# Kernel tuning notes

Measured on AMD Instinct MI355X. Metric: run time of the kernel, lower is better.

## Reference

```python
import jax, jax.numpy as jnp
from jax import lax
import numpy as np

N_POINTS = 1_000_000
K_STEPS = 32
N_FUNCS = 8
H = W = 1024
FID = 1000


def setup_inputs() -> dict:
    key = jax.random.key(0)
    ks = jax.random.split(key, 8)
    # palette: monotone 4-channel colormap-like table in [0,1]
    palette = jax.random.uniform(ks[0], (FID, 4), dtype=jnp.float32)
    # contractive-ish affine IFS so points stay mostly in frame
    A = 0.6 * jax.random.normal(ks[1], (N_FUNCS, 2, 2), dtype=jnp.float32)
    b = 0.8 * jax.random.normal(ks[2], (N_FUNCS, 2), dtype=jnp.float32)
    fcolor = jax.random.uniform(ks[3], (N_FUNCS,), dtype=jnp.float32)
    xy0 = jax.random.normal(ks[4], (N_POINTS, 2), dtype=jnp.float32)  # Normal(0, initial_sigma=1)
    c0 = jax.random.uniform(ks[5], (N_POINTS, 1), dtype=jnp.float32)
    fn_idx = jax.random.randint(ks[6], (K_STEPS, N_POINTS), 0, N_FUNCS, dtype=jnp.int32)
    # frame: x_left=-2, x_right=2, y_top=-2, y_bottom=2
    min_vec = jnp.array([[-2.0, -2.0]], dtype=jnp.float32)
    range_vec = jnp.array([[W / 4.0, H / 4.0]], dtype=jnp.float32)
    raw_image = jnp.zeros((4, H, W), dtype=jnp.float32)
    return {"raw_image": raw_image, "palette": palette, "A": A, "b": b,
            "fcolor": fcolor, "xy0": xy0, "c0": c0, "min_vec": min_vec,
            "range_vec": range_vec, "fn_idx": fn_idx, "skip_first_k": 4}


def reference(raw_image, palette, A, b, fcolor, xy0, c0, min_vec, range_vec, fn_idx, skip_first_k):
    height, width = raw_image.shape[1], raw_image.shape[2]
    fid = palette.shape[0]
    k_steps = fn_idx.shape[0]

    def step(carry, scanned):
        xy, c, img = carry
        idx, k = scanned
        # FunctionSet: per-point affine map + color blend
        xy = jnp.einsum('nij,nj->ni', A[idx], xy) + b[idx]          # [N,2]
        c = (c + fcolor[idx][:, None]) * 0.5                        # [N,1]
        colors = c[:, 0]
        pal_idx = (colors * (fid - 1) + 0.5 / fid).astype(jnp.int32)
        color_vectors = palette[jnp.clip(pal_idx, 0, fid - 1)]      # [N,4]
        bins = ((xy - min_vec) * range_vec).astype(jnp.int32)       # trunc toward 0, like .long()
        x_bins, y_bins = bins[:, 0], bins[:, 1]
        in_bounds = ((x_bins >= 0) & (x_bins < width) &
                     (y_bins >= 0) & (y_bins < height) & (k >= skip_first_k))
        vals = jnp.where(in_bounds[:, None], color_vectors, 0.0)    # [N,4]
        xb = jnp.clip(x_bins, 0, height - 1)  # source indexes img[c][x_bins, y_bins]
        yb = jnp.clip(y_bins, 0, width - 1)
        img = img.at[:, xb, yb].add(vals.T)
        return (xy, c, img), None

    (_, _, img), _ = lax.scan(step, (xy0, c0, raw_image),
                              (fn_idx, jnp.arange(k_steps)))
    return img
```

## Files before the change

### kernel.cpp

```cpp
#include <hip/hip_runtime.h>

typedef unsigned int u32;
typedef unsigned long long u64;

#define NPTS   1000000
#define KSTEPS 32
#define NF     8
#define IMG_H  1024
#define IMG_W  1024
#define FID    1000
#define HW     (IMG_H * IMG_W)
#define NB     3907
#define NBKT   512
#define BKTPX  2048
#define SEGW   (256 * KSTEPS)
#define K5G    1024
#define PARTCH 1016
#define PARTA_CH 488
#define MSTG   512
#define FPSCALE 4194304.0f
#define FPINV   (1.0f / 4194304.0f)

#define GETIDX(K)                                                              \
    ((int)(((((K) >> 3) == 0 ? p0 : ((K) >> 3) == 1 ? p1                       \
            : ((K) >> 3) == 2 ? p2 : p3) >> (((K) & 7) * 4)) & 7u))

#define FLAME_STEP(IDX, K)                                                     \
  {                                                                            \
    const float a00 = s_tab[(IDX)*8+0], a01 = s_tab[(IDX)*8+1];                \
    const float a10 = s_tab[(IDX)*8+2], a11 = s_tab[(IDX)*8+3];                \
    const float b0  = s_tab[(IDX)*8+4], b1  = s_tab[(IDX)*8+5];                \
    const float fc  = s_tab[(IDX)*8+6];                                        \
    const float nx = __fadd_rn(__fadd_rn(__fmul_rn(a00,x),__fmul_rn(a01,y)),b0);\
    const float ny = __fadd_rn(__fadd_rn(__fmul_rn(a10,x),__fmul_rn(a11,y)),b1);\
    x = nx; y = ny;                                                            \
    c = __fmul_rn(__fadd_rn(c, fc), 0.5f);                                     \
    xb = (int)__fmul_rn(__fsub_rn(x, minx), rx);                               \
    yb = (int)__fmul_rn(__fsub_rn(y, miny), ry);                               \
    inb = (xb >= 0) & (xb < IMG_W) & (yb >= 0) & (yb < IMG_H) & ((K) >= skipk);\
  }

#define LOAD_TABLES()                                                          \
    if (threadIdx.x < NF) {                                                    \
        const int f = threadIdx.x;                                             \
        s_tab[f*8+0] = Amat[f*4+0]; s_tab[f*8+1] = Amat[f*4+1];                \
        s_tab[f*8+2] = Amat[f*4+2]; s_tab[f*8+3] = Amat[f*4+3];                \
        s_tab[f*8+4] = bvec[f*2+0]; s_tab[f*8+5] = bvec[f*2+1];                \
        s_tab[f*8+6] = fcolor[f];   s_tab[f*8+7] = 0.0f;                       \
    }

__device__ __forceinline__ u32* part_ptr(u32* partA, u32* partB, u32 w) {
    return (w < PARTA_CH) ? partA + (size_t)w * (BKTPX * 4)
                          : partB + (size_t)(w - PARTA_CH) * (BKTPX * 4);
}
__device__ __forceinline__ const u32* part_ptr_c(const u32* partA,
                                                 const u32* partB, u32 w) {
    return (w < PARTA_CH) ? partA + (size_t)w * (BKTPX * 4)
                          : partB + (size_t)(w - PARTA_CH) * (BKTPX * 4);
}

__global__ __launch_bounds__(256) void k_flame(
    const float* __restrict__ Amat, const float* __restrict__ bvec,
    const float* __restrict__ fcolor,
    const float* __restrict__ xy0, const float* __restrict__ c0,
    const float* __restrict__ minv, const float* __restrict__ rangev,
    const int* __restrict__ fn_idx, const int* __restrict__ skipk_ptr,
    u32* __restrict__ counts, u32* __restrict__ lpre,
    u32* __restrict__ blockmajor)
{
    __shared__ u32 s_rec[SEGW];
    __shared__ u32 s_cnt[NBKT];
    __shared__ u32 s_scan[256];
    __shared__ float s_tab[NF * 8];
    const int tid = threadIdx.x;

    s_cnt[tid] = 0u; s_cnt[tid + 256] = 0u;
    LOAD_TABLES();
    __syncthreads();

    const int i = blockIdx.x * 256 + tid;
    u32 rec[KSTEPS];

    if (i < NPTS) {
        u32 p0 = 0, p1 = 0, p2 = 0, p3 = 0;
        #pragma unroll
        for (int k = 0; k < 8; ++k)
            p0 |= ((u32)fn_idx[(size_t)k * NPTS + i] & 7u) << (k * 4);
        #pragma unroll
        for (int k = 0; k < 8; ++k)
            p1 |= ((u32)fn_idx[(size_t)(k + 8) * NPTS + i] & 7u) << (k * 4);
        #pragma unroll
        for (int k = 0; k < 8; ++k)
            p2 |= ((u32)fn_idx[(size_t)(k + 16) * NPTS + i] & 7u) << (k * 4);
        #pragma unroll
        for (int k = 0; k < 8; ++k)
            p3 |= ((u32)fn_idx[(size_t)(k + 24) * NPTS + i] & 7u) << (k * 4);

        const int   skipk = skipk_ptr[0];
        const float minx = minv[0], miny = minv[1];
        const float rx = rangev[0], ry = rangev[1];
        const float2 xyv = ((const float2*)xy0)[i];
        float x = xyv.x, y = xyv.y, c = c0[i];
        #pragma unroll
        for (int k = 0; k < KSTEPS; ++k) {
            const int idx = GETIDX(k);
            int xb, yb; bool inb;
            FLAME_STEP(idx, k);
            u32 r = 0xFFFFFFFFu;
            if (inb) {
                int pi = (int)__fadd_rn(__fmul_rn(c, 999.0f), 0.0005f);
                pi = min(max(pi, 0), FID - 1);
                r = (((u32)(xb << 10 | yb)) << 10) | (u32)pi;
                atomicAdd(&s_cnt[r >> 21], 1u);
            }
            rec[k] = r;
        }
    }
    __syncthreads();

    const u32 cA = s_cnt[2 * tid], cB = s_cnt[2 * tid + 1];
    const u32 psum = cA + cB;
    s_scan[tid] = psum; __syncthreads();
    #pragma unroll
    for (int o = 1; o < 256; o <<= 1) {
        u32 t = (tid >= o) ? s_scan[tid - o] : 0u;
        __syncthreads();
        s_scan[tid] += t;
        __syncthreads();
    }
    const u32 excl = s_scan[tid] - psum;

    s_cnt[2 * tid] = excl; s_cnt[2 * tid + 1] = excl + cA;
    const size_t g0 = (size_t)blockIdx.x * NBKT;
    lpre[g0 + 2 * tid] = excl;  lpre[g0 + 2 * tid + 1] = excl + cA;
    counts[g0 + 2 * tid] = cA;  counts[g0 + 2 * tid + 1] = cB;
    __syncthreads();

    if (i < NPTS) {
        #pragma unroll
        for (int k = 0; k < KSTEPS; ++k) {
            const u32 r = rec[k];
            if (r != 0xFFFFFFFFu) {
                const u32 pos = atomicAdd(&s_cnt[r >> 21], 1u);
                s_rec[pos] = r;
            }
        }
    }
    __syncthreads();

    const u32 vt = s_scan[255];
    u32* dst = blockmajor + (size_t)blockIdx.x * SEGW;
    const u32 nv4 = vt >> 2;
    for (u32 q = tid; q < nv4; q += 256)
        ((uint4*)dst)[q] = make_uint4(s_rec[4*q], s_rec[4*q+1],
                                      s_rec[4*q+2], s_rec[4*q+3]);
    for (u32 j = (nv4 << 2) + tid; j < vt; j += 256) dst[j] = s_rec[j];
}

__global__ __launch_bounds__(256) void k_transpose(
    const u32* __restrict__ counts, const u32* __restrict__ lpre,
    u32* __restrict__ counts_t, u32* __restrict__ lpre_t,
    u32* __restrict__ totals)
{
    const int b = blockIdx.x, tid = threadIdx.x;
    u32 s = 0;
    for (int row = tid; row < NB; row += 256) {
        const u32 cv = counts[(size_t)row * NBKT + b];
        const u32 lv = lpre[(size_t)row * NBKT + b];
        counts_t[(size_t)b * NB + row] = cv;
        lpre_t[(size_t)b * NB + row] = lv;
        s += cv;
    }
    __shared__ u32 red[256];
    red[tid] = s; __syncthreads();
    #pragma unroll
    for (int o = 128; o; o >>= 1) {
        if (tid < o) red[tid] += red[tid + o];
        __syncthreads();
    }
    if (tid == 0) totals[b] = red[0];
}

__global__ __launch_bounds__(512) void k_meta(
    const float* __restrict__ palette,
    const u32* __restrict__ totals,
    u32* __restrict__ mm, u32* __restrict__ wstart,
    u32* __restrict__ pal_u32)
{
    __shared__ u32 sc[NBKT];
    const int tid = threadIdx.x;

    for (int t = tid; t < FID * 4; t += 512)
        pal_u32[t] = __float2uint_rn(__fmul_rn(palette[t], FPSCALE));

    const u32 t0 = totals[tid];
    sc[tid] = t0; __syncthreads();
    #pragma unroll
    for (int o = 1; o < NBKT; o <<= 1) {
        u32 v = (tid >= o) ? sc[tid - o] : 0u;
        __syncthreads(); sc[tid] += v; __syncthreads();
    }
    const u32 total = sc[NBKT - 1];

    const u32 m = 1u + (total ? (u32)((504ull * t0) / total) : 0u);
    mm[tid] = m;
    __syncthreads(); sc[tid] = m; __syncthreads();
    #pragma unroll
    for (int o = 1; o < NBKT; o <<= 1) {
        u32 v = (tid >= o) ? sc[tid - o] : 0u;
        __syncthreads(); sc[tid] += v; __syncthreads();
    }
    wstart[tid] = sc[tid] - m;
    if (tid == NBKT - 1) wstart[NBKT] = sc[NBKT - 1];
}

__global__ __launch_bounds__(512) void k_accum(
    const u32* __restrict__ pal_u32,
    const u32* __restrict__ counts_t, const u32* __restrict__ lpre_t,
    const u32* __restrict__ mm, const u32* __restrict__ wstart,
    const u32* __restrict__ blockmajor,
    u32* __restrict__ partA, u32* __restrict__ partB)
{
    __shared__ u64 tileA[BKTPX];
    __shared__ u64 tileB[BKTPX];
    __shared__ u32 s_ml[MSTG];
    __shared__ u32 s_pfx[MSTG + 1];
    __shared__ u32 s_ws[NBKT + 1];
    const int tid = threadIdx.x, w = blockIdx.x;

    if (tid < NBKT) s_ws[tid] = wstart[tid];
    if (tid == 0)   s_ws[NBKT] = wstart[NBKT];
    __syncthreads();
    if ((u32)w >= s_ws[NBKT]) return;

    int b = 0;
    #pragma unroll
    for (int step = 256; step; step >>= 1)
        if (b + step <= NBKT - 1 && s_ws[b + step] <= (u32)w) b += step;

    for (int t = tid; t < BKTPX; t += 512) { tileA[t] = 0ull; tileB[t] = 0ull; }

    const u32 m = mm[b], cch = (u32)w - s_ws[b];
    const u32 gs = (u32)(((u64)NB * cch) / m);
    const u32 ge = (u32)(((u64)NB * (cch + 1)) / m);

    const uint4* pal4 = (const uint4*)pal_u32;
    const u32* ct = counts_t + (size_t)b * NB;
    const u32* lt = lpre_t + (size_t)b * NB;

    for (u32 g0 = gs; g0 < ge; g0 += MSTG) {
        const u32 nm = min((u32)MSTG, ge - g0);
        __syncthreads();
        const u32 myc = (tid < (int)nm) ? ct[g0 + tid] : 0u;
        if (tid < (int)nm) s_ml[tid] = lt[g0 + tid];
        s_pfx[tid + 1] = myc;
        if (tid == 0) s_pfx[0] = 0u;
        __syncthreads();
        #pragma unroll
        for (int o = 1; o < MSTG; o <<= 1) {
            const u32 v = (tid >= o) ? s_pfx[tid - o + 1] : 0u;
            __syncthreads();
            s_pfx[tid + 1] += v;
            __syncthreads();
        }
        const u32 R = s_pfx[MSTG];

        u32 idx = (u32)tid;
        u32 r_c = 0;
        if (idx < R) {
            u32 g = 0;
            #pragma unroll
            for (int step = 256; step; step >>= 1)
                if (s_pfx[g + step] <= idx) g += step;
            r_c = blockmajor[(size_t)(g0 + g) * SEGW + s_ml[g] +
                             (idx - s_pfx[g])];
        }
        while (idx < R) {
            const u32 nidx = idx + 512;
            u32 r_n = 0;
            if (nidx < R) {
                u32 g = 0;
                #pragma unroll
                for (int step = 256; step; step >>= 1)
                    if (s_pfx[g + step] <= nidx) g += step;
                r_n = blockmajor[(size_t)(g0 + g) * SEGW + s_ml[g] +
                                 (nidx - s_pfx[g])];
            }
            const uint4 pc = pal4[r_c & 1023u];
            const u32 local = (r_c >> 10) & (BKTPX - 1);
            atomicAdd(&tileA[local], (u64)pc.x | ((u64)pc.y << 32));
            atomicAdd(&tileB[local], (u64)pc.z | ((u64)pc.w << 32));
            idx = nidx; r_c = r_n;
        }
    }
    __syncthreads();

    uint4* dst = (uint4*)part_ptr(partA, partB, (u32)w);
    for (int t = tid; t < BKTPX; t += 512)
        dst[t] = make_uint4((u32)tileA[t], (u32)(tileA[t] >> 32),
                            (u32)tileB[t], (u32)(tileB[t] >> 32));
}

__global__ __launch_bounds__(256) void k_final(
    const u32* __restrict__ partA, const u32* __restrict__ partB,
    const u32* __restrict__ wstart,
    const float* __restrict__ raw, float* __restrict__ out)
{
    const int p = blockIdx.x * 256 + threadIdx.x;
    const int b = p >> 11, local = p & (BKTPX - 1);
    u32 a0 = 0, a1 = 0, a2 = 0, a3 = 0;
    const u32 w0 = wstart[b], w1 = wstart[b + 1];
    for (u32 w = w0; w < w1; ++w) {
        const uint4 v = ((const uint4*)part_ptr_c(partA, partB, w))[local];
        a0 += v.x; a1 += v.y; a2 += v.z; a3 += v.w;
    }
    out[0*(size_t)HW + p] = __fadd_rn(raw[0*(size_t)HW + p], __fmul_rn((float)a0, FPINV));
    out[1*(size_t)HW + p] = __fadd_rn(raw[1*(size_t)HW + p], __fmul_rn((float)a1, FPINV));
    out[2*(size_t)HW + p] = __fadd_rn(raw[2*(size_t)HW + p], __fmul_rn((float)a2, FPINV));
    out[3*(size_t)HW + p] = __fadd_rn(raw[3*(size_t)HW + p], __fmul_rn((float)a3, FPINV));
}

__global__ __launch_bounds__(256) void flame_accum_packed(
    const float* __restrict__ palette,
    const float* __restrict__ Amat, const float* __restrict__ bvec,
    const float* __restrict__ fcolor,
    const float* __restrict__ xy0, const float* __restrict__ c0,
    const float* __restrict__ minv, const float* __restrict__ rangev,
    const int* __restrict__ fn_idx, const int* __restrict__ skipk_ptr,
    u64* __restrict__ ws)
{
    __shared__ __align__(16) float s_pal[FID * 4];
    __shared__ float s_tab[NF * 8];
    for (int t = threadIdx.x; t < FID; t += 256)
        ((float4*)s_pal)[t] = ((const float4*)palette)[t];
    LOAD_TABLES();
    __syncthreads();

    const int i = blockIdx.x * 256 + threadIdx.x;
    if (i >= NPTS) return;
    const int   skipk = skipk_ptr[0];
    const float minx = minv[0], miny = minv[1];
    const float rx = rangev[0], ry = rangev[1];
    const float2 xyv = ((const float2*)xy0)[i];
    float x = xyv.x, y = xyv.y, c = c0[i];
    for (int k = 0; k < KSTEPS; ++k) {
        const int idx = fn_idx[(size_t)k * NPTS + i];
        int xb, yb; bool inb;
        FLAME_STEP(idx, k);
        if (inb) {
            int pi = (int)__fadd_rn(__fmul_rn(c, 999.0f), 0.0005f);
            pi = min(max(pi, 0), FID - 1);
            const float4 col = *(const float4*)&s_pal[pi * 4];
            const u32 u0 = __float2uint_rn(__fmul_rn(col.x, FPSCALE));
            const u32 u1 = __float2uint_rn(__fmul_rn(col.y, FPSCALE));
            const u32 u2 = __float2uint_rn(__fmul_rn(col.z, FPSCALE));
            const u32 u3 = __float2uint_rn(__fmul_rn(col.w, FPSCALE));
            u64* p = ws + ((size_t)xb * IMG_W + yb) * 2;
            atomicAdd(p + 0, (u64)u0 | ((u64)u1 << 32));
            atomicAdd(p + 1, (u64)u2 | ((u64)u3 << 32));
        }
    }
}

__global__ __launch_bounds__(256) void reduce_packed(
    const u64* __restrict__ ws, const float* __restrict__ raw_image,
    float* __restrict__ out)
{
    const int p = blockIdx.x * 256 + threadIdx.x;
    if (p >= HW) return;
    const u64 w0 = ws[(size_t)p * 2 + 0];
    const u64 w1 = ws[(size_t)p * 2 + 1];
    out[0*(size_t)HW+p] = raw_image[0*(size_t)HW+p] + (float)(u32)(w0 & 0xffffffffull) * FPINV;
    out[1*(size_t)HW+p] = raw_image[1*(size_t)HW+p] + (float)(u32)(w0 >> 32)           * FPINV;
    out[2*(size_t)HW+p] = raw_image[2*(size_t)HW+p] + (float)(u32)(w1 & 0xffffffffull) * FPINV;
    out[3*(size_t)HW+p] = raw_image[3*(size_t)HW+p] + (float)(u32)(w1 >> 32)           * FPINV;
}

extern "C" void kernel_launch(void* const* d_in, const int* in_sizes, int n_in,
                              void* d_out, int out_size, void* d_ws, size_t ws_size,
                              hipStream_t stream) {
    const float* raw_image = (const float*)d_in[0];
    const float* palette   = (const float*)d_in[1];
    const float* A         = (const float*)d_in[2];
    const float* b         = (const float*)d_in[3];
    const float* fcolor    = (const float*)d_in[4];
    const float* xy0       = (const float*)d_in[5];
    const float* c0        = (const float*)d_in[6];
    const float* minv      = (const float*)d_in[7];
    const float* rangev    = (const float*)d_in[8];
    const int*   fn_idx    = (const int*)d_in[9];
    const int*   skipk     = (const int*)d_in[10];
    float* img = (float*)d_out;

    u32* ws = (u32*)d_ws;
    const size_t NBG = (size_t)NB * NBKT;
    u32* counts     = ws;
    u32* lpre       = counts + NBG;
    u32* counts_t   = lpre + NBG;
    u32* lpre_t     = counts_t + NBG;
    u32* totals     = lpre_t + NBG;
    u32* mm         = totals + NBKT;
    u32* wstart     = mm + NBKT;
    u32* pal_u32    = wstart + 1024;
    u32* blockmajor = pal_u32 + 4096;
    u32* partB      = blockmajor + (size_t)NB * SEGW;
    u32* partA      = counts;
    const size_t need_u32 = (size_t)(partB - ws) +
                            (size_t)(PARTCH - PARTA_CH) * (BKTPX * 4);
    const size_t NEED = need_u32 * sizeof(u32);

    if (ws_size >= NEED) {
        k_flame<<<dim3(NB), 256, 0, stream>>>(A, b, fcolor, xy0, c0, minv,
                                              rangev, fn_idx, skipk,
                                              counts, lpre, blockmajor);
        k_transpose<<<dim3(NBKT), 256, 0, stream>>>(counts, lpre,
                                                    counts_t, lpre_t, totals);
        k_meta<<<dim3(1), 512, 0, stream>>>(palette, totals, mm, wstart,
                                            pal_u32);
        k_accum<<<dim3(K5G), 512, 0, stream>>>(pal_u32, counts_t, lpre_t, mm,
                                               wstart, blockmajor,
                                               partA, partB);
        k_final<<<dim3(HW / 256), 256, 0, stream>>>(partA, partB, wstart,
                                                    raw_image, img);
    } else {
        const size_t need2 = (size_t)HW * 2 * sizeof(u64);
        hipMemsetAsync(d_ws, 0, need2, stream);
        flame_accum_packed<<<dim3(NB), 256, 0, stream>>>(
            palette, A, b, fcolor, xy0, c0, minv, rangev, fn_idx, skipk,
            (u64*)d_ws);
        reduce_packed<<<dim3((HW + 255) / 256), 256, 0, stream>>>(
            (const u64*)d_ws, raw_image, img);
    }
}
```

Measured before the change: 182.8 us.

## Split accumulation blocks by channel pair to halve LDS tiles and double grid

Each k_accum chunk now runs as two blocks, each handling two of the four color channels with a single u64 LDS tile instead of two. The grid doubles to 2048 and the partial tiles are stored per half, with k_final reading two uint2 partials per chunk. The aim is to halve LDS use per block for higher occupancy and more parallelism, at the cost of reading and binary-searching the record stream twice.

```diff
diff --git a/kernel.cpp b/kernel.cpp
--- a/kernel.cpp
+++ b/kernel.cpp
@@ -14,9 +14,11 @@
 #define NBKT   512
 #define BKTPX  2048
 #define SEGW   (256 * KSTEPS)
-#define K5G    1024
 #define PARTCH 1016
-#define PARTA_CH 488
+#define HTILES (2 * PARTCH)
+#define HTW    4096
+#define PARTA_T 976
+#define K5G2   2048
 #define MSTG   512
 #define FPSCALE 4194304.0f
 #define FPINV   (1.0f / 4194304.0f)
@@ -49,14 +51,14 @@
         s_tab[f*8+6] = fcolor[f];   s_tab[f*8+7] = 0.0f;                       \
     }
 
-__device__ __forceinline__ u32* part_ptr(u32* partA, u32* partB, u32 w) {
-    return (w < PARTA_CH) ? partA + (size_t)w * (BKTPX * 4)
-                          : partB + (size_t)(w - PARTA_CH) * (BKTPX * 4);
-}
-__device__ __forceinline__ const u32* part_ptr_c(const u32* partA,
-                                                 const u32* partB, u32 w) {
-    return (w < PARTA_CH) ? partA + (size_t)w * (BKTPX * 4)
-                          : partB + (size_t)(w - PARTA_CH) * (BKTPX * 4);
+__device__ __forceinline__ u32* htile_ptr(u32* partA, u32* partB, u32 h) {
+    return (h < PARTA_T) ? partA + (size_t)h * HTW
+                         : partB + (size_t)(h - PARTA_T) * HTW;
+}
+__device__ __forceinline__ const u32* htile_ptr_c(const u32* partA,
+                                                  const u32* partB, u32 h) {
+    return (h < PARTA_T) ? partA + (size_t)h * HTW
+                         : partB + (size_t)(h - PARTA_T) * HTW;
 }
 
 __global__ __launch_bounds__(256) void k_flame(
@@ -221,12 +223,14 @@
     const u32* __restrict__ blockmajor,
     u32* __restrict__ partA, u32* __restrict__ partB)
 {
-    __shared__ u64 tileA[BKTPX];
-    __shared__ u64 tileB[BKTPX];
+    __shared__ u64 tileH[BKTPX];
     __shared__ u32 s_ml[MSTG];
     __shared__ u32 s_pfx[MSTG + 1];
     __shared__ u32 s_ws[NBKT + 1];
-    const int tid = threadIdx.x, w = blockIdx.x;
+    const int tid = threadIdx.x;
+    const int half = (blockIdx.x >= PARTCH) ? 1 : 0;
+    const int w = blockIdx.x - half * PARTCH;
+    if (w >= PARTCH) return;
 
     if (tid < NBKT) s_ws[tid] = wstart[tid];
     if (tid == 0)   s_ws[NBKT] = wstart[NBKT];
@@ -238,13 +242,13 @@
     for (int step = 256; step; step >>= 1)
         if (b + step <= NBKT - 1 && s_ws[b + step] <= (u32)w) b += step;
 
-    for (int t = tid; t < BKTPX; t += 512) { tileA[t] = 0ull; tileB[t] = 0ull; }
+    for (int t = tid; t < BKTPX; t += 512) tileH[t] = 0ull;
 
     const u32 m = mm[b], cch = (u32)w - s_ws[b];
     const u32 gs = (u32)(((u64)NB * cch) / m);
     const u32 ge = (u32)(((u64)NB * (cch + 1)) / m);
 
-    const uint4* pal4 = (const uint4*)pal_u32;
+    const u32* palh = pal_u32 + half * 2;
     const u32* ct = counts_t + (size_t)b * NB;
     const u32* lt = lpre_t + (size_t)b * NB;
 
@@ -286,19 +290,19 @@
                 r_n = blockmajor[(size_t)(g0 + g) * SEGW + s_ml[g] +
                                  (nidx - s_pfx[g])];
             }
-            const uint4 pc = pal4[r_c & 1023u];
+            const u32 pb = (r_c & 1023u) * 4;
+            const u32 c0v = palh[pb], c1v = palh[pb + 1];
             const u32 local = (r_c >> 10) & (BKTPX - 1);
-            atomicAdd(&tileA[local], (u64)pc.x | ((u64)pc.y << 32));
-            atomicAdd(&tileB[local], (u64)pc.z | ((u64)pc.w << 32));
+            atomicAdd(&tileH[local], (u64)c0v | ((u64)c1v << 32));
             idx = nidx; r_c = r_n;
         }
     }
     __syncthreads();
 
-    uint4* dst = (uint4*)part_ptr(partA, partB, (u32)w);
+    u32* dst = htile_ptr(partA, partB, (u32)(half * PARTCH + w));
+    const uint2* src = (const uint2*)tileH;
     for (int t = tid; t < BKTPX; t += 512)
-        dst[t] = make_uint4((u32)tileA[t], (u32)(tileA[t] >> 32),
-                            (u32)tileB[t], (u32)(tileB[t] >> 32));
+        ((uint2*)dst)[t] = src[t];
 }
 
 __global__ __launch_bounds__(256) void k_final(
@@ -311,8 +315,10 @@
     u32 a0 = 0, a1 = 0, a2 = 0, a3 = 0;
     const u32 w0 = wstart[b], w1 = wstart[b + 1];
     for (u32 w = w0; w < w1; ++w) {
-        const uint4 v = ((const uint4*)part_ptr_c(partA, partB, w))[local];
-        a0 += v.x; a1 += v.y; a2 += v.z; a3 += v.w;
+        const uint2 vA = ((const uint2*)htile_ptr_c(partA, partB, w))[local];
+        const uint2 vB = ((const uint2*)htile_ptr_c(partA, partB,
+                                                    PARTCH + w))[local];
+        a0 += vA.x; a1 += vA.y; a2 += vB.x; a3 += vB.y;
     }
     out[0*(size_t)HW + p] = __fadd_rn(raw[0*(size_t)HW + p], __fmul_rn((float)a0, FPINV));
     out[1*(size_t)HW + p] = __fadd_rn(raw[1*(size_t)HW + p], __fmul_rn((float)a1, FPINV));
@@ -406,7 +412,7 @@
     u32* partB      = blockmajor + (size_t)NB * SEGW;
     u32* partA      = counts;
     const size_t need_u32 = (size_t)(partB - ws) +
-                            (size_t)(PARTCH - PARTA_CH) * (BKTPX * 4);
+                            (size_t)(HTILES - PARTA_T) * HTW;
     const size_t NEED = need_u32 * sizeof(u32);
 
     if (ws_size >= NEED) {
@@ -417,9 +423,9 @@
                                                     counts_t, lpre_t, totals);
         k_meta<<<dim3(1), 512, 0, stream>>>(palette, totals, mm, wstart,
                                             pal_u32);
-        k_accum<<<dim3(K5G), 512, 0, stream>>>(pal_u32, counts_t, lpre_t, mm,
-                                               wstart, blockmajor,
-                                               partA, partB);
+        k_accum<<<dim3(K5G2), 512, 0, stream>>>(pal_u32, counts_t, lpre_t, mm,
+                                                wstart, blockmajor,
+                                                partA, partB);
         k_final<<<dim3(HW / 256), 256, 0, stream>>>(partA, partB, wstart,
                                                     raw_image, img);
     } else {
```

New measurement: 233.5 us. +27.7%, slower.
